# Kernel optimization log

Measured on AMD Instinct MI355X. Metric: run time of the kernel, lower is better.

The kernel has to match this reference:

```python
import jax, jax.numpy as jnp
import numpy as np
from jax import lax

NR, NC, DI, DO = 2048, 10, 8, 16  # routes, digit caps, in-dim, out-dim

# (t1, a1, b1, a2, b2, t3, a3, b3, a4, b4) piecewise-affine squash constants
PRIM_CONSTS = (-13.46416092, 0.000242759, 0.024488359, 0.002769205, 0.06089699,
               13.23405266, -0.002828244, 0.061313814, -0.000219038, 0.023874787)
DIGIT_CONSTS = (-0.075410217, -0.074520095, 0.349297946, -0.534473989, 0.27196494,
                0.062207676, 0.637642944, 0.295330779, 0.169344703, 0.353784456)


def _piecewise(s, t1, a1, b1, a2, b2, t3, a3, b3, a4, b4):
    # Faithful to the torch loop: new_sorted aliases sorted, so each segment
    # count (i1,i2,i3) is computed on the PARTIALLY-MODIFIED array, and each
    # slice end is idx-1 (off-by-one in the source), last slice ends at n-1.
    n = s.shape[0]
    ar = jnp.arange(n)
    i1 = jnp.sum(s < t1)
    s = jnp.where(ar < i1 - 1, a1 * s + b1, s)
    i2 = jnp.sum(s < 0.0)
    s = jnp.where((ar >= i1) & (ar < i2 - 1), a2 * s + b2, s)
    i3 = jnp.sum(s < t3)
    s = jnp.where((ar >= i2) & (ar < i3 - 1), a3 * s + b3, s)
    s = jnp.where((ar >= i3) & (ar < n - 1), a4 * s + b4, s)
    return s


def _squash_map(x, consts):
    # sort -> piecewise-affine remap -> unsort (one row)
    idx = jnp.argsort(x)
    s = _piecewise(x[idx], *consts)
    return s[jnp.argsort(idx)]


def _conv(x, w, b, stride):
    y = lax.conv_general_dilated(x, w, (stride, stride), 'VALID',
                                 dimension_numbers=('NCHW', 'OIHW', 'NCHW'))
    return y + b[None, :, None, None]


def capsnet_forward(data, conv1_w, conv1_b, prim_w, prim_b, W_dc,
                    dec_w1, dec_b1, dec_w2, dec_b2, dec_w3, dec_b3):
    B = data.shape[0]
    x = jax.nn.relu(_conv(data, conv1_w, conv1_b, 1))          # (B,256,24,24)
    u = _conv(x, prim_w, prim_b, 2).reshape(B, NR, DI)          # (B,2048,8) : 8 caps x 32ch x 8x8
    mag = jax.vmap(lambda r: _squash_map(r, PRIM_CONSTS))(u[:, :, 0])  # (B,2048)
    u_sq = mag[:, :, None] * u                                  # PrimaryCaps.my_squash2
    u_hat = jnp.einsum('rcoi,bri->brco', W_dc, u_sq)            # (B,2048,10,16)

    b_ij = jnp.zeros((NR, NC), dtype=u_hat.dtype)               # routing logits
    for it in range(3):
        c_ij = jax.nn.softmax(b_ij, axis=0)                     # softmax over routes (dim=1 in torch)
        s_j = jnp.einsum('rc,brco->bco', c_ij, u_hat)           # (B,10,16)
        f = jax.vmap(lambda r: _squash_map(r, DIGIT_CONSTS))(s_j[:, :, 0])  # (B,10)
        # torch writes the remapped value back into s_j in place (view aliasing),
        # so component 0 of v_j is f*f while other components are f*s_j
        s_mod = s_j.at[:, :, 0].set(f)
        v_j = f[:, :, None] * s_mod                             # (B,10,16)
        if it < 2:
            a_ij = jnp.einsum('brco,bco->brc', u_hat, v_j)      # agreement
            b_ij = b_ij + a_ij.mean(axis=0)

    # Decoder (reconstruction head)
    classes = jnp.sqrt(jnp.sum(v_j ** 2, axis=2))               # (B,10)
    classes = jax.nn.softmax(classes, axis=0)                   # softmax over batch, as in source
    idx = jnp.argmax(classes, axis=1)                           # (B,)
    masked = jnp.eye(NC, dtype=v_j.dtype)[idx]                  # (B,10) one-hot
    t = (v_j * masked[:, :, None]).reshape(B, -1)               # (B,160)
    h = jax.nn.relu(t @ dec_w1.T + dec_b1)
    h = jax.nn.relu(h @ dec_w2.T + dec_b2)
    recon = jax.nn.sigmoid(h @ dec_w3.T + dec_b3)               # (B,1024) = 32*32*1
    # single-array output: [flattened digit caps | flattened reconstruction]
    return jnp.concatenate([v_j.reshape(B, -1), recon], axis=1)  # (B,1184)


def setup_inputs() -> dict:
    key = jax.random.key(0)
    ks = jax.random.split(key, 12)
    f32 = jnp.float32
    return {
        'data': jax.random.normal(ks[0], (100, 1, 32, 32), f32),
        'conv1_w': jax.random.normal(ks[1], (256, 1, 9, 9), f32) * (1.0 / 9.0),
        'conv1_b': jnp.zeros((256,), f32),
        'prim_w': jax.random.normal(ks[2], (256, 256, 9, 9), f32) * (1.0 / 144.0),
        'prim_b': jnp.zeros((256,), f32),
        'W_dc': jax.random.normal(ks[3], (2048, 10, 16, 8), f32) * 0.05,
        'dec_w1': jax.random.normal(ks[4], (512, 160), f32) * 0.079,
        'dec_b1': jnp.zeros((512,), f32),
        'dec_w2': jax.random.normal(ks[5], (1024, 512), f32) * 0.0442,
        'dec_b2': jnp.zeros((1024,), f32),
        'dec_w3': jax.random.normal(ks[6], (1024, 1024), f32) * 0.03125,
        'dec_b3': jnp.zeros((1024,), f32),
        'train_or_test': 0,
        'epch': 0,
    }


def reference(data, conv1_w, conv1_b, prim_w, prim_b, W_dc,
              dec_w1, dec_b1, dec_w2, dec_b2, dec_w3, dec_b3,
              train_or_test, epch):
    return capsnet_forward(data, conv1_w, conv1_b, prim_w, prim_b, W_dc,
                           dec_w1, dec_b1, dec_w2, dec_b2, dec_w3, dec_b3)
```

## Files before the change

kernel.cpp:

```cpp
#include <hip/hip_runtime.h>
#include <cstdint>
#include <cstddef>


#define BATCH 100

static const size_t OFF_WT   = 0;
static const size_t OFF_X1   = 5308416;
static const size_t OFF_PU   = 20054016;
static const size_t OFF_UHAT = 0;
static const size_t OFF_U    = 33161216;
static const size_t OFF_BIJ  = 32768000;
static const size_t OFF_CIJ  = 32788480;
static const size_t OFF_SP   = 32808960;
static const size_t OFF_VJ   = 33064960;
static const size_t OFF_IDX  = 33080960;
static const size_t OFF_H1   = 33081088;
static const size_t OFF_H2   = 33132288;

#define PT1f -13.46416092f
#define PA1f 0.000242759f
#define PB1f 0.024488359f
#define PA2f 0.002769205f
#define PB2f 0.06089699f
#define PT3f 13.23405266f
#define PA3f -0.002828244f
#define PB3f 0.061313814f
#define PA4f -0.000219038f
#define PB4f 0.023874787f

#define DT1f -0.075410217f
#define DA1f -0.074520095f
#define DB1f 0.349297946f
#define DA2f -0.534473989f
#define DB2f 0.27196494f
#define DT3f 0.062207676f
#define DA3f 0.637642944f
#define DB3f 0.295330779f
#define DA4f 0.169344703f
#define DB4f 0.353784456f

__global__ __launch_bounds__(256)
void k_transpose_w(const float* __restrict__ w, float* __restrict__ wt) {
  __shared__ float tile[64 * 82];
  int ci = blockIdx.x, co0 = blockIdx.y * 64, t = threadIdx.x;
  for (int f = t; f < 64 * 81; f += 256) {
    int col = f / 81, tap = f - col * 81;
    tile[col * 82 + tap] = w[(size_t)(co0 + col) * 20736 + (size_t)ci * 81 + tap];
  }
  __syncthreads();
  for (int g = t; g < 64 * 81; g += 256) {
    int tap = g / 64, col = g - tap * 64;
    wt[((size_t)ci * 81 + tap) * 256 + co0 + col] = tile[col * 82 + tap];
  }
}

__global__ __launch_bounds__(256)
void k_conv1(const float* __restrict__ data, const float* __restrict__ cw,
             const float* __restrict__ cb, float* __restrict__ x1) {
  __shared__ float img[1024];
  __shared__ float wl[81 * 32];
  int b = blockIdx.x, cg = blockIdx.y, t = threadIdx.x;
  for (int f = t; f < 1024; f += 256) img[f] = data[(size_t)b * 1024 + f];
  for (int f = t; f < 2592; f += 256) {
    int tap = f >> 5, c = f & 31;
    wl[f] = cw[(size_t)(cg * 32 + c) * 81 + tap];
  }
  __syncthreads();
  for (int task = t; task < 1152; task += 256) {
    int q = task % 144, cq = task / 144;
    int p0 = q * 4, oh = p0 / 24, ow0 = p0 % 24;
    float a[4][4];
#pragma unroll
    for (int i = 0; i < 4; ++i)
#pragma unroll
      for (int j = 0; j < 4; ++j) a[i][j] = 0.f;
    for (int kh = 0; kh < 9; ++kh) {
      const float* ir = &img[(oh + kh) * 32 + ow0];
      const float* wr = &wl[kh * 9 * 32 + cq * 4];
#pragma unroll
      for (int kw = 0; kw < 9; ++kw) {
        float4 wv = *(const float4*)(wr + kw * 32);
#pragma unroll
        for (int j = 0; j < 4; ++j) {
          float xv = ir[kw + j];
          a[0][j] = fmaf(wv.x, xv, a[0][j]);
          a[1][j] = fmaf(wv.y, xv, a[1][j]);
          a[2][j] = fmaf(wv.z, xv, a[2][j]);
          a[3][j] = fmaf(wv.w, xv, a[3][j]);
        }
      }
    }
#pragma unroll
    for (int cc = 0; cc < 4; ++cc) {
      int c = cg * 32 + cq * 4 + cc;
      float bias = cb[c];
      float4 o4 = make_float4(fmaxf(a[cc][0] + bias, 0.f), fmaxf(a[cc][1] + bias, 0.f),
                              fmaxf(a[cc][2] + bias, 0.f), fmaxf(a[cc][3] + bias, 0.f));
      *(float4*)&x1[((size_t)(b * 256 + c) * 24 + oh) * 24 + ow0] = o4;
    }
  }
}

__global__ __launch_bounds__(256, 5)
void k_prim(const float* __restrict__ x1, const float* __restrict__ wt,
            float* __restrict__ pu) {
  __shared__ float wsh[2 * 81 * 32];
  __shared__ float xsh[2 * 2 * 2 * 288];
  int t = threadIdx.x;
  int tb = t >> 7, tl = t & 127;
  int coq = tl >> 4, posq = tl & 15;
  int oh = posq >> 1, owq = posq & 1;
  int ci_base = blockIdx.x * 32, cog = blockIdx.y, bpair = blockIdx.z;
  int b = bpair * 2 + tb;

  float acc[4][4];
#pragma unroll
  for (int i = 0; i < 4; ++i)
#pragma unroll
    for (int j = 0; j < 4; ++j) acc[i][j] = 0.f;

#pragma unroll 1
  for (int ci0 = ci_base; ci0 < ci_base + 32; ci0 += 2) {
    __syncthreads();
    for (int f = t; f < 576; f += 256) {
      int tbj = f / 288, m = f - tbj * 288;
      int cil = m / 144, mm = m - cil * 144;
      int r = mm / 6, mq = mm - r * 6;
      float4 v = *(const float4*)&x1[((size_t)(bpair * 2 + tbj) * 256 + ci0 + cil) * 576 +
                                     r * 24 + mq * 4];
      float* eb = &xsh[((tbj * 2 + cil) * 2 + 0) * 288 + r * 12 + mq * 2];
      *(float2*)eb = make_float2(v.x, v.z);
      *(float2*)(eb + 288) = make_float2(v.y, v.w);
    }
    for (int f = t; f < 1296; f += 256) {
      int cil = f / 648, rem = f - cil * 648;
      int tap = rem >> 3, cq = rem & 7;
      float4 v = *(const float4*)&wt[((size_t)(ci0 + cil) * 81 + tap) * 256 +
                                     cog * 32 + cq * 4];
      *(float4*)&wsh[(cil * 81 + tap) * 32 + cq * 4] = v;
    }
    __syncthreads();
#pragma unroll
    for (int cil = 0; cil < 2; ++cil) {
      const float* xb0 = &xsh[((tb * 2 + cil) * 2 + 0) * 288 + owq * 4];
      const float* wb0 = &wsh[cil * 81 * 32 + coq * 4];
#pragma unroll
      for (int kh = 0; kh < 9; ++kh) {
        int r = 2 * oh + kh;
        const float* xe = xb0 + r * 12;
        float e[8], o8[8];
        *(float4*)&e[0]  = *(const float4*)xe;
        *(float4*)&e[4]  = *(const float4*)(xe + 4);
        *(float4*)&o8[0] = *(const float4*)(xe + 288);
        *(float4*)&o8[4] = *(const float4*)(xe + 292);
        const float* wr = wb0 + kh * 9 * 32;
#pragma unroll
        for (int kp = 0; kp < 5; ++kp) {
          float4 wv = *(const float4*)(wr + kp * 64);
#pragma unroll
          for (int j = 0; j < 4; ++j) {
            float xv = e[kp + j];
            acc[0][j] = fmaf(wv.x, xv, acc[0][j]);
            acc[1][j] = fmaf(wv.y, xv, acc[1][j]);
            acc[2][j] = fmaf(wv.z, xv, acc[2][j]);
            acc[3][j] = fmaf(wv.w, xv, acc[3][j]);
          }
        }
#pragma unroll
        for (int kp = 0; kp < 4; ++kp) {
          float4 wv = *(const float4*)(wr + 32 + kp * 64);
#pragma unroll
          for (int j = 0; j < 4; ++j) {
            float xv = o8[kp + j];
            acc[0][j] = fmaf(wv.x, xv, acc[0][j]);
            acc[1][j] = fmaf(wv.y, xv, acc[1][j]);
            acc[2][j] = fmaf(wv.z, xv, acc[2][j]);
            acc[3][j] = fmaf(wv.w, xv, acc[3][j]);
          }
        }
      }
    }
  }
  float* pp = pu + (((size_t)blockIdx.x * BATCH + b) * 2048 +
                    (cog * 32 + coq * 4) * 8 + oh) * 8 + owq * 4;
#pragma unroll
  for (int cc = 0; cc < 4; ++cc) {
    float4 o4 = make_float4(acc[cc][0], acc[cc][1], acc[cc][2], acc[cc][3]);
    *(float4*)(pp + cc * 64) = o4;
  }
}

__global__ __launch_bounds__(256)
void k_ured(const float* __restrict__ pu, const float* __restrict__ pb,
            float* __restrict__ u) {
  int g4 = blockIdx.x * 256 + threadIdx.x;
  if (g4 >= 409600) return;
  size_t g = (size_t)g4 * 4;
  const size_t S = 1638400;
  float4 s = *(const float4*)(pu + g);
#pragma unroll
  for (int k = 1; k < 8; ++k) {
    float4 p = *(const float4*)(pu + (size_t)k * S + g);
    s.x += p.x; s.y += p.y; s.z += p.z; s.w += p.w;
  }
  int r = (int)((g >> 3) & 2047);
  float bias = pb[r >> 3];
  float4 o = make_float4(s.x + bias, s.y + bias, s.z + bias, s.w + bias);
  *(float4*)(u + g) = o;
}

__global__ __launch_bounds__(256)
void k_squash(float* __restrict__ u) {
  __shared__ float kv[2048];
  __shared__ int kid[2048];
  __shared__ int red[256];
  int b = blockIdx.x, t = threadIdx.x;
  for (int r = t; r < 2048; r += 256) {
    kv[r] = u[((size_t)b * 2048 + r) * 8];
    kid[r] = r;
  }
  __syncthreads();
  for (int size = 2; size <= 2048; size <<= 1) {
    for (int stride = size >> 1; stride > 0; stride >>= 1) {
#pragma unroll 1
      for (int s = 0; s < 4; ++s) {
        int i = t + s * 256;
        int pos = 2 * i - (i & (stride - 1));
        int q = pos + stride;
        float va = kv[pos], vb = kv[q];
        int ia = kid[pos], ib = kid[q];
        bool gt = (va > vb) || (va == vb && ia > ib);
        bool up = ((pos & size) == 0);
        if (gt == up) { kv[pos] = vb; kv[q] = va; kid[pos] = ib; kid[q] = ia; }
      }
      __syncthreads();
    }
  }
  int loc = 0;
#pragma unroll
  for (int s = 0; s < 8; ++s) loc += (kv[t + s * 256] < PT1f) ? 1 : 0;
  red[t] = loc; __syncthreads();
  for (int off = 128; off; off >>= 1) { if (t < off) red[t] += red[t + off]; __syncthreads(); }
  int i1 = red[0]; __syncthreads();
  float m1v[8];
  loc = 0;
#pragma unroll
  for (int s = 0; s < 8; ++s) {
    int p = t + s * 256;
    float v = kv[p];
    float m = (p < i1 - 1) ? (PA1f * v + PB1f) : v;
    m1v[s] = m;
    loc += (m < 0.f) ? 1 : 0;
  }
  red[t] = loc; __syncthreads();
  for (int off = 128; off; off >>= 1) { if (t < off) red[t] += red[t + off]; __syncthreads(); }
  int i2 = red[0]; __syncthreads();
  float m2v[8];
  loc = 0;
#pragma unroll
  for (int s = 0; s < 8; ++s) {
    int p = t + s * 256;
    float m = (p >= i1 && p < i2 - 1) ? (PA2f * m1v[s] + PB2f) : m1v[s];
    m2v[s] = m;
    loc += (m < PT3f) ? 1 : 0;
  }
  red[t] = loc; __syncthreads();
  for (int off = 128; off; off >>= 1) { if (t < off) red[t] += red[t + off]; __syncthreads(); }
  int i3 = red[0]; __syncthreads();
#pragma unroll
  for (int s = 0; s < 8; ++s) {
    int p = t + s * 256;
    float m = m2v[s];
    m = (p >= i2 && p < i3 - 1) ? (PA3f * m + PB3f) : m;
    m = (p >= i3 && p < 2047) ? (PA4f * m + PB4f) : m;
    int rid = kid[p];
    float* row = u + ((size_t)b * 2048 + rid) * 8;
    float4 lo = *(float4*)row;
    float4 hi = *(float4*)(row + 4);
    lo.x *= m; lo.y *= m; lo.z *= m; lo.w *= m;
    hi.x *= m; hi.y *= m; hi.z *= m; hi.w *= m;
    *(float4*)row = lo;
    *(float4*)(row + 4) = hi;
  }
}

__global__ __launch_bounds__(192)
void k_uhat(const float* __restrict__ Wdc, const float* __restrict__ usq,
            float* __restrict__ uhat) {
  int t = threadIdx.x;
  if (t >= 160) return;
  int r0 = blockIdx.x * 8;
  for (int rl = 0; rl < 8; ++rl) {
    int r = r0 + rl;
    const float* wp = Wdc + ((size_t)r * 160 + t) * 8;
    float4 wa = *(const float4*)wp;
    float4 wb = *(const float4*)(wp + 4);
#pragma unroll 2
    for (int b = 0; b < BATCH; ++b) {
      const float* us = usq + ((size_t)b * 2048 + r) * 8;
      float v = us[0] * wa.x + us[1] * wa.y + us[2] * wa.z + us[3] * wa.w +
                us[4] * wb.x + us[5] * wb.y + us[6] * wb.z + us[7] * wb.w;
      uhat[((size_t)b * 2048 + r) * 160 + t] = v;
    }
  }
}

__global__ void k_zero(float* __restrict__ p, int n) {
  int i = blockIdx.x * blockDim.x + threadIdx.x;
  if (i < n) p[i] = 0.f;
}

__global__ __launch_bounds__(256)
void k_softc(const float* __restrict__ bij, float* __restrict__ cij) {
  __shared__ float red[256];
  int c = blockIdx.x, t = threadIdx.x;
  float m = -3.402823466e38f;
  for (int r = t; r < 2048; r += 256) m = fmaxf(m, bij[r * 10 + c]);
  red[t] = m; __syncthreads();
  for (int off = 128; off; off >>= 1) { if (t < off) red[t] = fmaxf(red[t], red[t + off]); __syncthreads(); }
  m = red[0]; __syncthreads();
  float s = 0.f;
  for (int r = t; r < 2048; r += 256) s += expf(bij[r * 10 + c] - m);
  red[t] = s; __syncthreads();
  for (int off = 128; off; off >>= 1) { if (t < off) red[t] += red[t + off]; __syncthreads(); }
  s = red[0];
  for (int r = t; r < 2048; r += 256) cij[r * 10 + c] = expf(bij[r * 10 + c] - m) / s;
}

__global__ __launch_bounds__(192)
void k_sjpart(const float* __restrict__ cij, const float* __restrict__ uhat,
              float* __restrict__ sp) {
  __shared__ float cl[1280];
  int b = blockIdx.x, ch = blockIdx.y, t = threadIdx.x;
  for (int f = t; f < 1280; f += 192) cl[f] = cij[(size_t)ch * 1280 + f];
  __syncthreads();
  if (t < 160) {
    int c = t >> 4;
    float acc = 0.f;
    const float* up = uhat + ((size_t)b * 2048 + ch * 128) * 160 + t;
#pragma unroll 4
    for (int rl = 0; rl < 128; ++rl) acc += cl[rl * 10 + c] * up[(size_t)rl * 160];
    sp[((size_t)b * 16 + ch) * 160 + t] = acc;
  }
}

__global__ __launch_bounds__(192)
void k_sjred(const float* __restrict__ sp, float* __restrict__ vj,
             float* __restrict__ dout, int finalit) {
  __shared__ float sl[160];
  __shared__ float fl[10];
  int b = blockIdx.x, t = threadIdx.x;
  if (t < 160) {
    float a = 0.f;
#pragma unroll
    for (int ch = 0; ch < 16; ++ch) a += sp[((size_t)b * 16 + ch) * 160 + t];
    sl[t] = a;
  }
  __syncthreads();
  if (t == 0) {
    float sv[10]; int rk[10];
    for (int c = 0; c < 10; ++c) sv[c] = sl[c * 16];
    for (int c = 0; c < 10; ++c) {
      int r = 0;
      for (int k = 0; k < 10; ++k)
        r += ((sv[k] < sv[c]) || (sv[k] == sv[c] && k < c)) ? 1 : 0;
      rk[c] = r;
    }
    int i1 = 0;
    for (int c = 0; c < 10; ++c) i1 += (sv[c] < DT1f) ? 1 : 0;
    float m1[10];
    for (int c = 0; c < 10; ++c) m1[c] = (rk[c] < i1 - 1) ? (DA1f * sv[c] + DB1f) : sv[c];
    int i2 = 0;
    for (int c = 0; c < 10; ++c) i2 += (m1[c] < 0.f) ? 1 : 0;
    float m2[10];
    for (int c = 0; c < 10; ++c)
      m2[c] = (rk[c] >= i1 && rk[c] < i2 - 1) ? (DA2f * m1[c] + DB2f) : m1[c];
    int i3 = 0;
    for (int c = 0; c < 10; ++c) i3 += (m2[c] < DT3f) ? 1 : 0;
    for (int c = 0; c < 10; ++c) {
      float m = (rk[c] >= i2 && rk[c] < i3 - 1) ? (DA3f * m2[c] + DB3f) : m2[c];
      m = (rk[c] >= i3 && rk[c] < 9) ? (DA4f * m + DB4f) : m;
      fl[c] = m;
    }
  }
  __syncthreads();
  if (t < 160) {
    int c = t >> 4, o = t & 15;
    float fv = fl[c];
    float v = fv * ((o == 0) ? fv : sl[t]);
    vj[(size_t)b * 160 + t] = v;
    if (finalit) dout[(size_t)b * 1184 + t] = v;
  }
}

__global__ __launch_bounds__(192)
void k_amean(const float* __restrict__ uhat, const float* __restrict__ vj,
             float* __restrict__ bij) {
  __shared__ float vl[16000];
  int t = threadIdx.x, r0 = blockIdx.x * 8;
  for (int f = t; f < 16000; f += 192) vl[f] = vj[f];
  __syncthreads();
  if (t < 160) {
    int c = t >> 4;
    for (int rl = 0; rl < 8; ++rl) {
      int r = r0 + rl;
      float acc = 0.f;
      const float* up = uhat + (size_t)r * 160 + t;
#pragma unroll 4
      for (int b = 0; b < BATCH; ++b) acc += up[(size_t)b * 2048 * 160] * vl[b * 160 + t];
      for (int off = 8; off; off >>= 1) acc += __shfl_down(acc, off, 16);
      if ((t & 15) == 0) bij[r * 10 + c] += acc / 100.0f;
    }
  }
}

__global__ __launch_bounds__(256)
void k_cls(const float* __restrict__ vj, int* __restrict__ idxg) {
  __shared__ float cl[1000];
  __shared__ float cm[10];
  __shared__ float cs[10];
  int t = threadIdx.x;
  for (int f = t; f < 1000; f += 256) {
    int b = f / 10, c = f - b * 10;
    float s = 0.f;
#pragma unroll
    for (int o = 0; o < 16; ++o) {
      float v = vj[(size_t)b * 160 + c * 16 + o];
      s += v * v;
    }
    cl[f] = sqrtf(s);
  }
  __syncthreads();
  if (t < 10) {
    float m = -3.402823466e38f;
    for (int b = 0; b < BATCH; ++b) m = fmaxf(m, cl[b * 10 + t]);
    float s = 0.f;
    for (int b = 0; b < BATCH; ++b) s += expf(cl[b * 10 + t] - m);
    cm[t] = m; cs[t] = s;
  }
  __syncthreads();
  for (int b = t; b < BATCH; b += 256) {
    float best = -1.f; int bi = 0;
    for (int c = 0; c < 10; ++c) {
      float val = expf(cl[b * 10 + c] - cm[c]) / cs[c];
      if (val > best) { best = val; bi = c; }
    }
    idxg[b] = bi;
  }
}

__global__ __launch_bounds__(256)
void k_dec1(const float* __restrict__ w1, const float* __restrict__ b1,
            const float* __restrict__ vj, const int* __restrict__ idxg,
            float* __restrict__ h1) {
  int b = blockIdx.x, t = threadIdx.x;
  int id = idxg[b];
  const float* v = vj + (size_t)b * 160 + id * 16;
  for (int j = t; j < 512; j += 256) {
    float acc = b1[j];
    const float* wr = w1 + (size_t)j * 160 + id * 16;
#pragma unroll
    for (int o = 0; o < 16; ++o) acc += wr[o] * v[o];
    h1[(size_t)b * 512 + j] = fmaxf(acc, 0.f);
  }
}

__global__ __launch_bounds__(256)
void k_dec2(const float* __restrict__ w2, const float* __restrict__ b2,
            const float* __restrict__ h1, float* __restrict__ h2) {
  __shared__ float red[4][64][4];
  int t = threadIdx.x, lane = t & 63, strip = t >> 6;
  int j = blockIdx.x * 64 + lane, bs = blockIdx.y * 4;
  float acc[4] = {0.f, 0.f, 0.f, 0.f};
  const float* wr = w2 + (size_t)j * 512 + strip * 128;
  const float* hb = h1 + (size_t)bs * 512 + strip * 128;
  for (int k4 = 0; k4 < 32; ++k4) {
    float4 wv = *(const float4*)(wr + k4 * 4);
    const float* h0 = hb + k4 * 4;
#pragma unroll
    for (int q = 0; q < 4; ++q) {
      float4 hv = *(const float4*)(h0 + q * 512);
      acc[q] += wv.x * hv.x + wv.y * hv.y + wv.z * hv.z + wv.w * hv.w;
    }
  }
#pragma unroll
  for (int q = 0; q < 4; ++q) red[strip][lane][q] = acc[q];
  __syncthreads();
  if (strip == 0) {
    float bias = b2[j];
#pragma unroll
    for (int q = 0; q < 4; ++q) {
      float tot = red[0][lane][q] + red[1][lane][q] + red[2][lane][q] + red[3][lane][q] + bias;
      h2[(size_t)(bs + q) * 1024 + j] = fmaxf(tot, 0.f);
    }
  }
}

__global__ __launch_bounds__(256)
void k_dec3(const float* __restrict__ w3, const float* __restrict__ b3,
            const float* __restrict__ h2, float* __restrict__ dout) {
  __shared__ float red[4][64][4];
  int t = threadIdx.x, lane = t & 63, strip = t >> 6;
  int j = blockIdx.x * 64 + lane, bs = blockIdx.y * 4;
  float acc[4] = {0.f, 0.f, 0.f, 0.f};
  const float* wr = w3 + (size_t)j * 1024 + strip * 256;
  const float* hb = h2 + (size_t)bs * 1024 + strip * 256;
  for (int k4 = 0; k4 < 64; ++k4) {
    float4 wv = *(const float4*)(wr + k4 * 4);
    const float* h0 = hb + k4 * 4;
#pragma unroll
    for (int q = 0; q < 4; ++q) {
      float4 hv = *(const float4*)(h0 + q * 1024);
      acc[q] += wv.x * hv.x + wv.y * hv.y + wv.z * hv.z + wv.w * hv.w;
    }
  }
#pragma unroll
  for (int q = 0; q < 4; ++q) red[strip][lane][q] = acc[q];
  __syncthreads();
  if (strip == 0) {
    float bias = b3[j];
#pragma unroll
    for (int q = 0; q < 4; ++q) {
      float tot = red[0][lane][q] + red[1][lane][q] + red[2][lane][q] + red[3][lane][q] + bias;
      dout[(size_t)(bs + q) * 1184 + 160 + j] = 1.f / (1.f + expf(-tot));
    }
  }
}

extern "C" void kernel_launch(void* const* d_in, const int* in_sizes, int n_in,
                              void* d_out, int out_size, void* d_ws, size_t ws_size,
                              hipStream_t stream) {
  (void)in_sizes; (void)n_in; (void)out_size; (void)ws_size;
  const float* data = (const float*)d_in[0];
  const float* c1w  = (const float*)d_in[1];
  const float* c1b  = (const float*)d_in[2];
  const float* pw   = (const float*)d_in[3];
  const float* pb   = (const float*)d_in[4];
  const float* Wdc  = (const float*)d_in[5];
  const float* w1   = (const float*)d_in[6];
  const float* b1   = (const float*)d_in[7];
  const float* w2   = (const float*)d_in[8];
  const float* b2   = (const float*)d_in[9];
  const float* w3   = (const float*)d_in[10];
  const float* b3   = (const float*)d_in[11];
  float* out = (float*)d_out;
  float* ws  = (float*)d_ws;

  float* WT   = ws + OFF_WT;
  float* X1   = ws + OFF_X1;
  float* PU   = ws + OFF_PU;
  float* UHAT = ws + OFF_UHAT;
  float* U    = ws + OFF_U;
  float* BIJ  = ws + OFF_BIJ;
  float* CIJ  = ws + OFF_CIJ;
  float* SP   = ws + OFF_SP;
  float* VJ   = ws + OFF_VJ;
  int*   IDX  = (int*)(ws + OFF_IDX);
  float* H1   = ws + OFF_H1;
  float* H2   = ws + OFF_H2;

  k_transpose_w<<<dim3(256, 4), 256, 0, stream>>>(pw, WT);
  k_conv1<<<dim3(BATCH, 8), 256, 0, stream>>>(data, c1w, c1b, X1);
  k_prim<<<dim3(8, 8, 50), 256, 0, stream>>>(X1, WT, PU);
  k_ured<<<1600, 256, 0, stream>>>(PU, pb, U);
  k_squash<<<BATCH, 256, 0, stream>>>(U);
  k_uhat<<<256, 192, 0, stream>>>(Wdc, U, UHAT);
  k_zero<<<80, 256, 0, stream>>>(BIJ, 20480);

  for (int it = 0; it < 3; ++it) {
    k_softc<<<10, 256, 0, stream>>>(BIJ, CIJ);
    k_sjpart<<<dim3(BATCH, 16), 192, 0, stream>>>(CIJ, UHAT, SP);
    k_sjred<<<BATCH, 192, 0, stream>>>(SP, VJ, out, it == 2 ? 1 : 0);
    if (it < 2) k_amean<<<256, 192, 0, stream>>>(UHAT, VJ, BIJ);
  }

  k_cls<<<1, 256, 0, stream>>>(VJ, IDX);
  k_dec1<<<BATCH, 256, 0, stream>>>(w1, b1, VJ, IDX, H1);
  k_dec2<<<dim3(16, 25), 256, 0, stream>>>(w2, b2, H1, H2);
  k_dec3<<<dim3(16, 25), 256, 0, stream>>>(w3, b3, H2, out);
}
```

Baseline: 1.544 ms.

## Retile primary-caps conv per block and skip first-iteration routing softmax

The primary-capsule convolution now gives each block four batch images and each thread a full 8-wide output row per channel quad (32 accumulators). It loads one input channel per stage instead of two, so weight reads from shared memory are reused across more outputs and the grid shrinks by half. Separately, the first routing iteration uses the known uniform coupling (1/2048) instead of zeroing b_ij and running softmax. The first agreement update then writes b_ij directly, which removes the zero kernel and one softmax launch. The conv change raises register pressure and halves the single-channel stage depth per sync, which may hurt occupancy.

```diff
diff --git a/kernel.cpp b/kernel.cpp
--- a/kernel.cpp
+++ b/kernel.cpp
@@ -105,89 +105,85 @@
 __global__ __launch_bounds__(256, 5)
 void k_prim(const float* __restrict__ x1, const float* __restrict__ wt,
             float* __restrict__ pu) {
-  __shared__ float wsh[2 * 81 * 32];
-  __shared__ float xsh[2 * 2 * 2 * 288];
+  __shared__ float wsh[81 * 32];
+  __shared__ float xsh[4 * 2 * 288];
   int t = threadIdx.x;
-  int tb = t >> 7, tl = t & 127;
-  int coq = tl >> 4, posq = tl & 15;
-  int oh = posq >> 1, owq = posq & 1;
-  int ci_base = blockIdx.x * 32, cog = blockIdx.y, bpair = blockIdx.z;
-  int b = bpair * 2 + tb;
-
-  float acc[4][4];
+  int tb = t >> 6, tl = t & 63;
+  int coq = tl >> 3, oh = tl & 7;
+  int ci_base = blockIdx.x * 32, cog = blockIdx.y, bq = blockIdx.z;
+  int b = bq * 4 + tb;
+
+  float acc[4][8];
 #pragma unroll
   for (int i = 0; i < 4; ++i)
 #pragma unroll
-    for (int j = 0; j < 4; ++j) acc[i][j] = 0.f;
+    for (int j = 0; j < 8; ++j) acc[i][j] = 0.f;
 
 #pragma unroll 1
-  for (int ci0 = ci_base; ci0 < ci_base + 32; ci0 += 2) {
+  for (int ci = ci_base; ci < ci_base + 32; ++ci) {
     __syncthreads();
-    for (int f = t; f < 576; f += 256) {
-      int tbj = f / 288, m = f - tbj * 288;
-      int cil = m / 144, mm = m - cil * 144;
-      int r = mm / 6, mq = mm - r * 6;
-      float4 v = *(const float4*)&x1[((size_t)(bpair * 2 + tbj) * 256 + ci0 + cil) * 576 +
-                                     r * 24 + mq * 4];
-      float* eb = &xsh[((tbj * 2 + cil) * 2 + 0) * 288 + r * 12 + mq * 2];
-      *(float2*)eb = make_float2(v.x, v.z);
-      *(float2*)(eb + 288) = make_float2(v.y, v.w);
-    }
-    for (int f = t; f < 1296; f += 256) {
-      int cil = f / 648, rem = f - cil * 648;
-      int tap = rem >> 3, cq = rem & 7;
-      float4 v = *(const float4*)&wt[((size_t)(ci0 + cil) * 81 + tap) * 256 +
-                                     cog * 32 + cq * 4];
-      *(float4*)&wsh[(cil * 81 + tap) * 32 + cq * 4] = v;
+    for (int f = t; f < 288; f += 256) {
+      int tbj = f / 72, rem = f - tbj * 72;
+      int r = rem / 3, oct = rem - r * 3;
+      const float* gp = &x1[((size_t)(bq * 4 + tbj) * 256 + ci) * 576 + r * 24 + oct * 8];
+      float4 v1 = *(const float4*)gp;
+      float4 v2 = *(const float4*)(gp + 4);
+      float* eb = &xsh[tbj * 576 + r * 12 + oct * 4];
+      *(float4*)eb = make_float4(v1.x, v1.z, v2.x, v2.z);
+      *(float4*)(eb + 288) = make_float4(v1.y, v1.w, v2.y, v2.w);
+    }
+    for (int f = t; f < 648; f += 256) {
+      int tap = f >> 3, cq = f & 7;
+      float4 v = *(const float4*)&wt[((size_t)ci * 81 + tap) * 256 + cog * 32 + cq * 4];
+      *(float4*)&wsh[tap * 32 + cq * 4] = v;
     }
     __syncthreads();
-#pragma unroll
-    for (int cil = 0; cil < 2; ++cil) {
-      const float* xb0 = &xsh[((tb * 2 + cil) * 2 + 0) * 288 + owq * 4];
-      const float* wb0 = &wsh[cil * 81 * 32 + coq * 4];
-#pragma unroll
-      for (int kh = 0; kh < 9; ++kh) {
-        int r = 2 * oh + kh;
-        const float* xe = xb0 + r * 12;
-        float e[8], o8[8];
-        *(float4*)&e[0]  = *(const float4*)xe;
-        *(float4*)&e[4]  = *(const float4*)(xe + 4);
-        *(float4*)&o8[0] = *(const float4*)(xe + 288);
-        *(float4*)&o8[4] = *(const float4*)(xe + 292);
-        const float* wr = wb0 + kh * 9 * 32;
-#pragma unroll
-        for (int kp = 0; kp < 5; ++kp) {
-          float4 wv = *(const float4*)(wr + kp * 64);
-#pragma unroll
-          for (int j = 0; j < 4; ++j) {
-            float xv = e[kp + j];
-            acc[0][j] = fmaf(wv.x, xv, acc[0][j]);
-            acc[1][j] = fmaf(wv.y, xv, acc[1][j]);
-            acc[2][j] = fmaf(wv.z, xv, acc[2][j]);
-            acc[3][j] = fmaf(wv.w, xv, acc[3][j]);
-          }
-        }
-#pragma unroll
-        for (int kp = 0; kp < 4; ++kp) {
-          float4 wv = *(const float4*)(wr + 32 + kp * 64);
-#pragma unroll
-          for (int j = 0; j < 4; ++j) {
-            float xv = o8[kp + j];
-            acc[0][j] = fmaf(wv.x, xv, acc[0][j]);
-            acc[1][j] = fmaf(wv.y, xv, acc[1][j]);
-            acc[2][j] = fmaf(wv.z, xv, acc[2][j]);
-            acc[3][j] = fmaf(wv.w, xv, acc[3][j]);
-          }
+    const float* xb = &xsh[tb * 576];
+    const float* wb = &wsh[coq * 4];
+#pragma unroll 3
+    for (int kh = 0; kh < 9; ++kh) {
+      int r = 2 * oh + kh;
+      const float* xe = xb + r * 12;
+      float ew[12], ov[12];
+      *(float4*)&ew[0] = *(const float4*)xe;
+      *(float4*)&ew[4] = *(const float4*)(xe + 4);
+      *(float4*)&ew[8] = *(const float4*)(xe + 8);
+      *(float4*)&ov[0] = *(const float4*)(xe + 288);
+      *(float4*)&ov[4] = *(const float4*)(xe + 292);
+      *(float4*)&ov[8] = *(const float4*)(xe + 296);
+      const float* wr = wb + kh * 9 * 32;
+#pragma unroll
+      for (int p = 0; p < 5; ++p) {
+        float4 wv = *(const float4*)(wr + p * 64);
+#pragma unroll
+        for (int j = 0; j < 8; ++j) {
+          float xv = ew[p + j];
+          acc[0][j] = fmaf(wv.x, xv, acc[0][j]);
+          acc[1][j] = fmaf(wv.y, xv, acc[1][j]);
+          acc[2][j] = fmaf(wv.z, xv, acc[2][j]);
+          acc[3][j] = fmaf(wv.w, xv, acc[3][j]);
         }
       }
+#pragma unroll
+      for (int p = 0; p < 4; ++p) {
+        float4 wv = *(const float4*)(wr + 32 + p * 64);
+#pragma unroll
+        for (int j = 0; j < 8; ++j) {
+          float xv = ov[p + j];
+          acc[0][j] = fmaf(wv.x, xv, acc[0][j]);
+          acc[1][j] = fmaf(wv.y, xv, acc[1][j]);
+          acc[2][j] = fmaf(wv.z, xv, acc[2][j]);
+          acc[3][j] = fmaf(wv.w, xv, acc[3][j]);
+        }
+      }
     }
   }
   float* pp = pu + (((size_t)blockIdx.x * BATCH + b) * 2048 +
-                    (cog * 32 + coq * 4) * 8 + oh) * 8 + owq * 4;
+                    (cog * 32 + coq * 4) * 8 + oh) * 8;
 #pragma unroll
   for (int cc = 0; cc < 4; ++cc) {
-    float4 o4 = make_float4(acc[cc][0], acc[cc][1], acc[cc][2], acc[cc][3]);
-    *(float4*)(pp + cc * 64) = o4;
+    *(float4*)(pp + cc * 64)     = make_float4(acc[cc][0], acc[cc][1], acc[cc][2], acc[cc][3]);
+    *(float4*)(pp + cc * 64 + 4) = make_float4(acc[cc][4], acc[cc][5], acc[cc][6], acc[cc][7]);
   }
 }
 
@@ -306,11 +302,6 @@
   }
 }
 
-__global__ void k_zero(float* __restrict__ p, int n) {
-  int i = blockIdx.x * blockDim.x + threadIdx.x;
-  if (i < n) p[i] = 0.f;
-}
-
 __global__ __launch_bounds__(256)
 void k_softc(const float* __restrict__ bij, float* __restrict__ cij) {
   __shared__ float red[256];
@@ -330,17 +321,25 @@
 
 __global__ __launch_bounds__(192)
 void k_sjpart(const float* __restrict__ cij, const float* __restrict__ uhat,
-              float* __restrict__ sp) {
+              float* __restrict__ sp, int it0) {
   __shared__ float cl[1280];
   int b = blockIdx.x, ch = blockIdx.y, t = threadIdx.x;
-  for (int f = t; f < 1280; f += 192) cl[f] = cij[(size_t)ch * 1280 + f];
+  if (!it0) {
+    for (int f = t; f < 1280; f += 192) cl[f] = cij[(size_t)ch * 1280 + f];
+  }
   __syncthreads();
   if (t < 160) {
     int c = t >> 4;
     float acc = 0.f;
     const float* up = uhat + ((size_t)b * 2048 + ch * 128) * 160 + t;
+    if (it0) {
+      const float cuni = 0.00048828125f;
 #pragma unroll 4
-    for (int rl = 0; rl < 128; ++rl) acc += cl[rl * 10 + c] * up[(size_t)rl * 160];
+      for (int rl = 0; rl < 128; ++rl) acc += cuni * up[(size_t)rl * 160];
+    } else {
+#pragma unroll 4
+      for (int rl = 0; rl < 128; ++rl) acc += cl[rl * 10 + c] * up[(size_t)rl * 160];
+    }
     sp[((size_t)b * 16 + ch) * 160 + t] = acc;
   }
 }
@@ -396,7 +395,7 @@
 
 __global__ __launch_bounds__(192)
 void k_amean(const float* __restrict__ uhat, const float* __restrict__ vj,
-             float* __restrict__ bij) {
+             float* __restrict__ bij, int first) {
   __shared__ float vl[16000];
   int t = threadIdx.x, r0 = blockIdx.x * 8;
   for (int f = t; f < 16000; f += 192) vl[f] = vj[f];
@@ -410,7 +409,10 @@
 #pragma unroll 4
       for (int b = 0; b < BATCH; ++b) acc += up[(size_t)b * 2048 * 160] * vl[b * 160 + t];
       for (int off = 8; off; off >>= 1) acc += __shfl_down(acc, off, 16);
-      if ((t & 15) == 0) bij[r * 10 + c] += acc / 100.0f;
+      if ((t & 15) == 0) {
+        float val = acc / 100.0f;
+        bij[r * 10 + c] = first ? val : (bij[r * 10 + c] + val);
+      }
     }
   }
 }
@@ -562,17 +564,16 @@
 
   k_transpose_w<<<dim3(256, 4), 256, 0, stream>>>(pw, WT);
   k_conv1<<<dim3(BATCH, 8), 256, 0, stream>>>(data, c1w, c1b, X1);
-  k_prim<<<dim3(8, 8, 50), 256, 0, stream>>>(X1, WT, PU);
+  k_prim<<<dim3(8, 8, 25), 256, 0, stream>>>(X1, WT, PU);
   k_ured<<<1600, 256, 0, stream>>>(PU, pb, U);
   k_squash<<<BATCH, 256, 0, stream>>>(U);
   k_uhat<<<256, 192, 0, stream>>>(Wdc, U, UHAT);
-  k_zero<<<80, 256, 0, stream>>>(BIJ, 20480);
 
   for (int it = 0; it < 3; ++it) {
-    k_softc<<<10, 256, 0, stream>>>(BIJ, CIJ);
-    k_sjpart<<<dim3(BATCH, 16), 192, 0, stream>>>(CIJ, UHAT, SP);
+    if (it > 0) k_softc<<<10, 256, 0, stream>>>(BIJ, CIJ);
+    k_sjpart<<<dim3(BATCH, 16), 192, 0, stream>>>(CIJ, UHAT, SP, it == 0 ? 1 : 0);
     k_sjred<<<BATCH, 192, 0, stream>>>(SP, VJ, out, it == 2 ? 1 : 0);
-    if (it < 2) k_amean<<<256, 192, 0, stream>>>(UHAT, VJ, BIJ);
+    if (it < 2) k_amean<<<256, 192, 0, stream>>>(UHAT, VJ, BIJ, it == 0 ? 1 : 0);
   }
 
   k_cls<<<1, 256, 0, stream>>>(VJ, IDX);
```

Result: faster. 1.460 ms (-5.5%).
